# Kernel optimization log

Hardware: AMD Instinct MI355X
Metric: run time of the kernel (lower is better)

Reference implementation:

```python
import jax, jax.numpy as jnp
import numpy as np

NUM_HEADS = 8
EMBED_DIM = 512
MAX_SEQ = 2048
HEAD_DIM = EMBED_DIM // NUM_HEADS
B, S = 2, 2048


def setup_inputs() -> dict:
    key = jax.random.key(0)
    ks = jax.random.split(key, 12)
    sd = 1.0 / np.sqrt(EMBED_DIM)
    return {
        "q_in": jax.random.normal(ks[0], (B, S, EMBED_DIM), jnp.float32),
        "k_in": jax.random.normal(ks[1], (B, S, EMBED_DIM), jnp.float32),
        "v_in": jax.random.normal(ks[2], (B, S, EMBED_DIM), jnp.float32),
        "Wq": jax.random.normal(ks[3], (EMBED_DIM, EMBED_DIM), jnp.float32) * sd,
        "bq": jnp.zeros((EMBED_DIM,), jnp.float32),
        "Wk": jax.random.normal(ks[4], (EMBED_DIM, EMBED_DIM), jnp.float32) * sd,
        "bk": jnp.zeros((EMBED_DIM,), jnp.float32),
        "Wv": jax.random.normal(ks[5], (EMBED_DIM, EMBED_DIM), jnp.float32) * sd,
        "bv": jnp.zeros((EMBED_DIM,), jnp.float32),
        "Wo": jax.random.normal(ks[6], (EMBED_DIM, EMBED_DIM), jnp.float32) * sd,
        "bo": jnp.zeros((EMBED_DIM,), jnp.float32),
        "rel_emb": jax.random.normal(ks[7], (MAX_SEQ, HEAD_DIM), jnp.float32) * sd,
    }


def _split_heads(x, W, b):
    # x: [B,S,E] -> [B,H,S,D]
    y = x @ W + b
    b_, s_ = y.shape[0], y.shape[1]
    return y.reshape(b_, s_, NUM_HEADS, HEAD_DIM).transpose(0, 2, 1, 3)


def _relative_scores(q, rel_emb):
    # q: [B,H,L,D]; rel_emb sliced to last L rows: [M,D] with M == L here
    L = q.shape[2]
    rel = rel_emb[max(0, MAX_SEQ - L):, :]
    M = rel.shape[0]
    scores = jnp.einsum('bhld,md->bhlm', q, rel)
    # mask = flip(tri(L,M), axis=-1): zero out future relative positions
    mask = jnp.flip(jnp.tri(L, M, dtype=jnp.float32), axis=1)
    scores = scores * mask
    # skew trick: pad one column on the left, reshape swapping last two dims, drop first row
    padded = jnp.pad(scores, ((0, 0), (0, 0), (0, 0), (1, 0)))  # [B,H,L,M+1]
    reshaped = padded.reshape(padded.shape[0], padded.shape[1], M + 1, L)
    skewed = reshaped[:, :, 1:, :]  # [B,H,M,L] == [B,H,L,L]
    return skewed


def reference(q_in, k_in, v_in, Wq, bq, Wk, bk, Wv, bv, Wo, bo, rel_emb):
    q = _split_heads(q_in, Wq, bq)  # [B,H,S,D]
    k = _split_heads(k_in, Wk, bk)
    v = _split_heads(v_in, Wv, bv)
    scores = jnp.einsum('bhqd,bhkd->bhqk', q, k)
    rel_scores = _relative_scores(q, rel_emb)
    logits = (scores + rel_scores) / jnp.sqrt(jnp.float32(HEAD_DIM))
    attn = jax.nn.softmax(logits, axis=-1)
    out = jnp.einsum('bhqk,bhkd->bhqd', attn, v)  # [B,H,S,D]
    merged = out.transpose(0, 2, 1, 3).reshape(out.shape[0], -1, EMBED_DIM)
    return merged @ Wo + bo, attn
```

## Files before the change

kernel.cpp:

```cpp
#include <hip/hip_runtime.h>


typedef __attribute__((ext_vector_type(4))) float f32x4;
typedef __attribute__((ext_vector_type(8))) short short8;

__device__ inline unsigned short f2bf(float x) {
    unsigned u = __float_as_uint(x);
    unsigned r = (u + 0x7fffu + ((u >> 16) & 1u)) >> 16;
    return (unsigned short)r;
}
__device__ inline float bf2f(unsigned short h) {
    return __uint_as_float(((unsigned)h) << 16);
}
__device__ inline int swz(int row, int bytecol) {
    return (row << 7) + (bytecol ^ ((row & 7) << 4));
}
__device__ inline void cvt4(float4 v, uint2& hi, uint2& lo) {
    unsigned short h0 = f2bf(v.x), h1 = f2bf(v.y), h2 = f2bf(v.z), h3 = f2bf(v.w);
    hi = make_uint2(((unsigned)h1 << 16) | h0, ((unsigned)h3 << 16) | h2);
    lo = make_uint2(((unsigned)f2bf(v.y - bf2f(h1)) << 16) | f2bf(v.x - bf2f(h0)),
                    ((unsigned)f2bf(v.w - bf2f(h3)) << 16) | f2bf(v.z - bf2f(h2)));
}
__device__ inline uint2 cvt4hi(float4 v) {
    return make_uint2(((unsigned)f2bf(v.y) << 16) | f2bf(v.x),
                      ((unsigned)f2bf(v.w) << 16) | f2bf(v.z));
}

__global__ __launch_bounds__(256) void wt_prep4(const float* __restrict__ W0,
                                                const float* __restrict__ W1,
                                                const float* __restrict__ W2,
                                                const float* __restrict__ W3,
                                                unsigned short* __restrict__ wt)
{
    __shared__ float Ls[32][33];
    const int t = threadIdx.x;
    const int z = blockIdx.z;
    const float* W = (z == 0) ? W0 : (z == 1) ? W1 : (z == 2) ? W2 : W3;
    unsigned short* WTh = wt + (size_t)(2 * z) * 262144;
    unsigned short* WTl = wt + (size_t)(2 * z + 1) * 262144;
    const int k0 = blockIdx.x << 5, n0 = blockIdx.y << 5;
#pragma unroll
    for (int i = 0; i < 4; ++i) {
        int idx = (i << 8) + t;
        int kk = idx >> 5, nn = idx & 31;
        Ls[kk][nn] = W[(size_t)(k0 + kk) * 512 + n0 + nn];
    }
    __syncthreads();
#pragma unroll
    for (int i = 0; i < 2; ++i) {
        int idx = (i << 8) + t;
        int nn = idx >> 4, kp = idx & 15;
        float f0 = Ls[2 * kp][nn], f1 = Ls[2 * kp + 1][nn];
        unsigned short h0 = f2bf(f0), h1 = f2bf(f1);
        size_t off = (size_t)(n0 + nn) * 512 + k0 + 2 * kp;
        *(unsigned*)&WTh[off] = ((unsigned)h1 << 16) | h0;
        *(unsigned*)&WTl[off] = ((unsigned)f2bf(f1 - bf2f(h1)) << 16) | f2bf(f0 - bf2f(h0));
    }
}

__global__ __launch_bounds__(256) void rel_prep(const float* __restrict__ rel,
                                                unsigned short* __restrict__ relh)
{
    int idx = (blockIdx.x * 256 + threadIdx.x) << 3;
    float4 a = *(const float4*)&rel[idx];
    float4 b = *(const float4*)&rel[idx + 4];
    uint4 o;
    o.x = ((unsigned)f2bf(a.y) << 16) | f2bf(a.x);
    o.y = ((unsigned)f2bf(a.w) << 16) | f2bf(a.z);
    o.z = ((unsigned)f2bf(b.y) << 16) | f2bf(b.x);
    o.w = ((unsigned)f2bf(b.w) << 16) | f2bf(b.z);
    *(uint4*)&relh[idx] = o;
}

__device__ __forceinline__ void gemm64_core(const float* __restrict__ A,
                                            const unsigned short* __restrict__ WTh,
                                            const unsigned short* __restrict__ WTl,
                                            int m0, int n0, char* smem, int t,
                                            f32x4 (&acc)[4])
{
    char* aH = smem;
    char* aL = smem + 8192;
    char* wH = smem + 16384;
    char* wL = smem + 24576;
    const int lane = t & 63, w = t >> 6;
    const int lr = lane & 15, kg = lane >> 4;

    for (int k0 = 0; k0 < 512; k0 += 64) {
        if (k0) __syncthreads();
#pragma unroll
        for (int i = 0; i < 4; ++i) {
            int idx = (i << 8) + t;
            int row = idx >> 4, c4 = idx & 15;
            float4 v = *(const float4*)&A[(size_t)(m0 + row) * 512 + k0 + (c4 << 2)];
            uint2 hi, lo; cvt4(v, hi, lo);
            int ph = swz(row, c4 << 3);
            *(uint2*)(aH + ph) = hi;
            *(uint2*)(aL + ph) = lo;
        }
#pragma unroll
        for (int i = 0; i < 4; ++i) {
            int idx = (i << 8) + t;
            int plane = idx >> 9, rem = idx & 511;
            int nn = rem >> 3, j8 = rem & 7;
            const unsigned short* src = plane ? WTl : WTh;
            uint4 vv = *(const uint4*)&src[(size_t)(n0 + nn) * 512 + k0 + (j8 << 3)];
            *(uint4*)((plane ? wL : wH) + swz(nn, j8 << 4)) = vv;
        }
        __syncthreads();
#pragma unroll
        for (int kk = 0; kk < 2; ++kk) {
            int bc = (kk << 6) + (kg << 4);
            int ar = (w << 4) + lr;
            short8 a_h = *(const short8*)(aH + swz(ar, bc));
            short8 a_l = *(const short8*)(aL + swz(ar, bc));
#pragma unroll
            for (int f = 0; f < 4; ++f) {
                short8 b_h = *(const short8*)(wH + swz((f << 4) + lr, bc));
                short8 b_l = *(const short8*)(wL + swz((f << 4) + lr, bc));
                acc[f] = __builtin_amdgcn_mfma_f32_16x16x32_bf16(a_h, b_h, acc[f], 0, 0, 0);
                acc[f] = __builtin_amdgcn_mfma_f32_16x16x32_bf16(a_l, b_h, acc[f], 0, 0, 0);
                acc[f] = __builtin_amdgcn_mfma_f32_16x16x32_bf16(a_h, b_l, acc[f], 0, 0, 0);
            }
        }
    }
}

__global__ __launch_bounds__(256) void gemm_qkv(
    const float* __restrict__ Aq, const float* __restrict__ Ak, const float* __restrict__ Av,
    const unsigned short* __restrict__ wt,
    const float* __restrict__ bq, const float* __restrict__ bk, const float* __restrict__ bv,
    unsigned short* __restrict__ qh, unsigned short* __restrict__ ql,
    unsigned short* __restrict__ kh, unsigned short* __restrict__ kl,
    unsigned short* __restrict__ vh, unsigned short* __restrict__ vl)
{
    __shared__ char smem[32768];
    const int t = threadIdx.x;
    const int z = blockIdx.z;
    const int n0 = blockIdx.x << 6;
    const int m0 = blockIdx.y << 6;
    const int lane = t & 63, w = t >> 6;
    const int lr = lane & 15, kg = lane >> 4;

    const float* A = (z == 0) ? Aq : (z == 1) ? Ak : Av;
    const float* bias = (z == 0) ? bq : (z == 1) ? bk : bv;
    const unsigned short* WTh = wt + (size_t)(2 * z) * 262144;
    const unsigned short* WTl = wt + (size_t)(2 * z + 1) * 262144;
    unsigned short* outH = (z == 0) ? qh : (z == 1) ? kh : vh;
    unsigned short* outL = (z == 0) ? ql : (z == 1) ? kl : vl;

    f32x4 acc[4];
#pragma unroll
    for (int f = 0; f < 4; ++f) acc[f] = {0.f, 0.f, 0.f, 0.f};

    gemm64_core(A, WTh, WTl, m0, n0, smem, t, acc);

    const int mbase = m0 + (w << 4) + (kg << 2);
    const int b = mbase >> 11, s = mbase & 2047;
    const int bidx = (b << 3) + (n0 >> 6);
#pragma unroll
    for (int f = 0; f < 4; ++f) {
        int d = (f << 4) + lr;
        float bv_ = bias[n0 + d];
        if (z < 2) {
#pragma unroll
            for (int e = 0; e < 4; ++e) {
                float val = acc[f][e] + bv_;
                unsigned short hh = f2bf(val);
                size_t off = ((size_t)bidx * 2048 + s + e) * 64 + d;
                outH[off] = hh;
                outL[off] = f2bf(val - bf2f(hh));
            }
        } else {
            unsigned short h[4], l[4];
#pragma unroll
            for (int e = 0; e < 4; ++e) {
                float val = acc[f][e] + bv_;
                h[e] = f2bf(val);
                l[e] = f2bf(val - bf2f(h[e]));
            }
            size_t off = ((size_t)bidx * 64 + d) * 2048 + s;
            *(uint2*)&outH[off] = make_uint2(((unsigned)h[1] << 16) | h[0],
                                             ((unsigned)h[3] << 16) | h[2]);
            *(uint2*)&outL[off] = make_uint2(((unsigned)l[1] << 16) | l[0],
                                             ((unsigned)l[3] << 16) | l[2]);
        }
    }
}

__global__ __launch_bounds__(256) void gemm_out(
    const float* __restrict__ pO,
    const unsigned short* __restrict__ WTh, const unsigned short* __restrict__ WTl,
    const float* __restrict__ bias, float* __restrict__ out0)
{
    __shared__ char smem[32768];
    char* aH = smem;
    char* aL = smem + 8192;
    char* wH = smem + 16384;
    char* wL = smem + 24576;
    const int t = threadIdx.x;
    const int n0 = blockIdx.x << 6;
    const int m0 = blockIdx.y << 6;
    const int lane = t & 63, w = t >> 6;
    const int lr = lane & 15, kg = lane >> 4;
    const int bq = m0 >> 11, s0 = m0 & 2047;

    f32x4 acc[4];
#pragma unroll
    for (int f = 0; f < 4; ++f) acc[f] = {0.f, 0.f, 0.f, 0.f};

    for (int k0 = 0; k0 < 512; k0 += 64) {
        if (k0) __syncthreads();
        const float* p0 = pO + ((size_t)((bq << 3) + (k0 >> 6)) * 2048 + s0) * 64;
#pragma unroll
        for (int i = 0; i < 2; ++i) {
            int idx = (i << 8) + t;
            int row = idx >> 3, j8 = idx & 7;
            size_t off = (size_t)row * 64 + (j8 << 3);
            float4 a0 = *(const float4*)&p0[off];
            float4 a1 = *(const float4*)&p0[off + 4];
            float4 b0 = *(const float4*)&p0[off + 2097152];
            float4 b1 = *(const float4*)&p0[off + 4 + 2097152];
            float4 v0 = make_float4(a0.x + b0.x, a0.y + b0.y, a0.z + b0.z, a0.w + b0.w);
            float4 v1 = make_float4(a1.x + b1.x, a1.y + b1.y, a1.z + b1.z, a1.w + b1.w);
            uint2 h0, l0, h1, l1;
            cvt4(v0, h0, l0);
            cvt4(v1, h1, l1);
            int ph = swz(row, j8 << 4);
            *(uint4*)(aH + ph) = make_uint4(h0.x, h0.y, h1.x, h1.y);
            *(uint4*)(aL + ph) = make_uint4(l0.x, l0.y, l1.x, l1.y);
        }
#pragma unroll
        for (int i = 0; i < 4; ++i) {
            int idx = (i << 8) + t;
            int plane = idx >> 9, rem = idx & 511;
            int nn = rem >> 3, j8 = rem & 7;
            const unsigned short* src = plane ? WTl : WTh;
            uint4 vv = *(const uint4*)&src[(size_t)(n0 + nn) * 512 + k0 + (j8 << 3)];
            *(uint4*)((plane ? wL : wH) + swz(nn, j8 << 4)) = vv;
        }
        __syncthreads();
#pragma unroll
        for (int kk = 0; kk < 2; ++kk) {
            int bc = (kk << 6) + (kg << 4);
            int ar = (w << 4) + lr;
            short8 a_h = *(const short8*)(aH + swz(ar, bc));
            short8 a_l = *(const short8*)(aL + swz(ar, bc));
#pragma unroll
            for (int f = 0; f < 4; ++f) {
                short8 b_h = *(const short8*)(wH + swz((f << 4) + lr, bc));
                short8 b_l = *(const short8*)(wL + swz((f << 4) + lr, bc));
                acc[f] = __builtin_amdgcn_mfma_f32_16x16x32_bf16(a_h, b_h, acc[f], 0, 0, 0);
                acc[f] = __builtin_amdgcn_mfma_f32_16x16x32_bf16(a_l, b_h, acc[f], 0, 0, 0);
                acc[f] = __builtin_amdgcn_mfma_f32_16x16x32_bf16(a_h, b_l, acc[f], 0, 0, 0);
            }
        }
    }

    const int mbase = m0 + (w << 4) + (kg << 2);
#pragma unroll
    for (int f = 0; f < 4; ++f) {
        int n = n0 + (f << 4) + lr;
        float bv = bias[n];
#pragma unroll
        for (int e = 0; e < 4; ++e)
            out0[(size_t)(mbase + e) * 512 + n] = acc[f][e] + bv;
    }
}

__global__ __launch_bounds__(512, 4) void logits_flash(
    const unsigned short* __restrict__ qh_g, const unsigned short* __restrict__ ql_g,
    const unsigned short* __restrict__ kh_g, const unsigned short* __restrict__ kl_g,
    const unsigned short* __restrict__ relh_g,
    float* __restrict__ attn, unsigned short* __restrict__ rawh,
    float* __restrict__ tilemax, int mode,
    float2* __restrict__ stats)
{
    __shared__ char smem[59136];
    char* kh = smem;
    char* kl = smem + 16384;
    char* bandP = smem + 32768;
    unsigned short* Pt = (unsigned short*)(smem + 32768);
    float* part_m = (float*)(smem + 58112);
    float* part_z = (float*)(smem + 58624);

    const int t = threadIdx.x;
    const int bh = blockIdx.y;
    int ib = blockIdx.x; if (bh & 8) ib = 31 - ib;
    const int i0 = ib << 6;
    const int lane = t & 63, w = t >> 6;
    const int wr = w >> 1, wc = w & 1;
    const int lr = lane & 15, kg = lane >> 4;
    const int irow = (wr << 4) + lr;

    const size_t qoff = ((size_t)bh * 2048 + i0 + irow) * 64;
    const short8 aH0 = *(const short8*)(qh_g + qoff + (kg << 3));
    const short8 aH1 = *(const short8*)(qh_g + qoff + 32 + (kg << 3));
    const short8 aL0 = *(const short8*)(ql_g + qoff + (kg << 3));
    const short8 aL1 = *(const short8*)(ql_g + qoff + 32 + (kg << 3));

    float rm = -3.0e38f, rz = 0.f;

    const unsigned short* khb = kh_g + (size_t)bh * 2048 * 64;
    const unsigned short* klb = kl_g + (size_t)bh * 2048 * 64;
    const size_t obase = ((size_t)bh * 2048 + i0) * 2048;

    for (int jt = 0; jt < 16; ++jt) {
        const int j0 = jt << 7;
        const bool anyRel = (j0 <= i0 + 63);
        const int m0 = 1984 - i0 + j0;
        __syncthreads();
        if (jt > 0 && t < 64) {
            float m1 = part_m[t], m2 = part_m[64 + t];
            float z1 = part_z[t], z2 = part_z[64 + t];
            float tm = fmaxf(m1, m2);
            float tz = z1 * __expf((m1 - tm) * 0.125f) + z2 * __expf((m2 - tm) * 0.125f);
            float mn = fmaxf(rm, tm);
            rz = rz * __expf((rm - mn) * 0.125f) + tz * __expf((tm - mn) * 0.125f);
            rm = mn;
        }
        {
            int rr = t >> 2, gp = (t & 3) << 1;
            const unsigned short* s0 = khb + (size_t)(j0 + rr) * 64 + (gp << 3);
            *(uint4*)(kh + swz(rr, gp << 4)) = *(const uint4*)s0;
            *(uint4*)(kh + swz(rr, (gp + 1) << 4)) = *(const uint4*)(s0 + 8);
            const unsigned short* s1 = klb + (size_t)(j0 + rr) * 64 + (gp << 3);
            *(uint4*)(kl + swz(rr, gp << 4)) = *(const uint4*)s1;
            *(uint4*)(kl + swz(rr, (gp + 1) << 4)) = *(const uint4*)(s1 + 8);
        }
        if (anyRel) {
#pragma unroll
            for (int i = 0; i < 3; ++i) {
                int idx = (i << 9) + t;
                int row = idx >> 3, g = idx & 7;
                int m = m0 + row; if (m > 2047) m = 2047;
                *(uint4*)(bandP + swz(row, g << 4)) = *(const uint4*)(relh_g + (size_t)m * 64 + (g << 3));
            }
        }
        __syncthreads();

        f32x4 acc[4];
#pragma unroll
        for (int cf = 0; cf < 4; ++cf) {
            int krow = (wc << 6) + (cf << 4) + lr;
            short8 bH0 = *(const short8*)(kh + swz(krow, kg << 4));
            short8 bH1 = *(const short8*)(kh + swz(krow, 64 + (kg << 4)));
            short8 bL0 = *(const short8*)(kl + swz(krow, kg << 4));
            short8 bL1 = *(const short8*)(kl + swz(krow, 64 + (kg << 4)));
            f32x4 c = {0.f, 0.f, 0.f, 0.f};
            c = __builtin_amdgcn_mfma_f32_16x16x32_bf16(bH0, aH0, c, 0, 0, 0);
            c = __builtin_amdgcn_mfma_f32_16x16x32_bf16(bH1, aH1, c, 0, 0, 0);
            c = __builtin_amdgcn_mfma_f32_16x16x32_bf16(bH0, aL0, c, 0, 0, 0);
            c = __builtin_amdgcn_mfma_f32_16x16x32_bf16(bH1, aL1, c, 0, 0, 0);
            c = __builtin_amdgcn_mfma_f32_16x16x32_bf16(bL0, aH0, c, 0, 0, 0);
            c = __builtin_amdgcn_mfma_f32_16x16x32_bf16(bL1, aH1, c, 0, 0, 0);
            acc[cf] = c;
        }
        if (anyRel) {
            f32x4 pr[6];
#pragma unroll
            for (int q = 0; q < 6; ++q) {
                int ff = (wc ? 6 : 0) + q;
                int brow = (ff << 4) + lr;
                short8 rb0 = *(const short8*)(bandP + swz(brow, kg << 4));
                short8 rb1 = *(const short8*)(bandP + swz(brow, 64 + (kg << 4)));
                f32x4 c = {0.f, 0.f, 0.f, 0.f};
                c = __builtin_amdgcn_mfma_f32_16x16x32_bf16(rb0, aH0, c, 0, 0, 0);
                c = __builtin_amdgcn_mfma_f32_16x16x32_bf16(rb1, aH1, c, 0, 0, 0);
                pr[q] = c;
            }
            __syncthreads();
#pragma unroll
            for (int q = 0; q < 6; ++q) {
                int ff = (wc ? 6 : 0) + q;
#pragma unroll
                for (int e = 0; e < 4; ++e)
                    Pt[((ff << 4) + (kg << 2) + e) * 66 + irow] = f2bf(pr[q][e]);
            }
            __syncthreads();
        }

        float rowmax = -3.0e38f;
#pragma unroll
        for (int cf = 0; cf < 4; ++cf) {
            int jl0 = (wc << 6) + (cf << 4) + (kg << 2);
            f32x4 a = acc[cf];
#pragma unroll
            for (int e = 0; e < 4; ++e) {
                int jl = jl0 + e;
                if (anyRel && (jl - irow) <= (i0 - j0))
                    a[e] += bf2f(Pt[(jl + 63 - irow) * 66 + irow]);
            }
            acc[cf] = a;
            rowmax = fmaxf(rowmax, fmaxf(fmaxf(a[0], a[1]), fmaxf(a[2], a[3])));
        }
        rowmax = fmaxf(rowmax, __shfl_xor(rowmax, 16, 64));
        rowmax = fmaxf(rowmax, __shfl_xor(rowmax, 32, 64));

        float zs = 0.f;
#pragma unroll
        for (int cf = 0; cf < 4; ++cf) {
            int jl0 = (wc << 6) + (cf << 4) + (kg << 2);
            f32x4 a = acc[cf];
            f32x4 u;
#pragma unroll
            for (int e = 0; e < 4; ++e) {
                u[e] = __expf((a[e] - rowmax) * 0.125f);
                zs += u[e];
            }
            size_t oidx = obase + (size_t)irow * 2048 + j0 + jl0;
            if (mode == 2) {
                *(uint2*)&rawh[oidx] = make_uint2(
                    (unsigned)f2bf(u[0]) | ((unsigned)f2bf(u[1]) << 16),
                    (unsigned)f2bf(u[2]) | ((unsigned)f2bf(u[3]) << 16));
            } else if (mode == 1) {
                *(uint2*)&rawh[oidx] = make_uint2(
                    (unsigned)f2bf(a[0]) | ((unsigned)f2bf(a[1]) << 16),
                    (unsigned)f2bf(a[2]) | ((unsigned)f2bf(a[3]) << 16));
            } else {
                *(float4*)&attn[oidx] = make_float4(a[0], a[1], a[2], a[3]);
            }
        }
        zs += __shfl_xor(zs, 16, 64);
        zs += __shfl_xor(zs, 32, 64);
        if (lane < 16) {
            part_m[(wc << 6) + irow] = rowmax;
            part_z[(wc << 6) + irow] = zs;
            if (mode == 2)
                tilemax[(size_t)((jt << 1) + wc) * 32768 + bh * 2048 + i0 + irow] = rowmax;
        }
    }
    __syncthreads();
    if (t < 64) {
        float m1 = part_m[t], m2 = part_m[64 + t];
        float z1 = part_z[t], z2 = part_z[64 + t];
        float tm = fmaxf(m1, m2);
        float tz = z1 * __expf((m1 - tm) * 0.125f) + z2 * __expf((m2 - tm) * 0.125f);
        float mn = fmaxf(rm, tm);
        rz = rz * __expf((rm - mn) * 0.125f) + tz * __expf((tm - mn) * 0.125f);
        rm = mn;
        stats[bh * 2048 + i0 + t] = make_float2(rm, 1.0f / rz);
    }
}

__global__ __launch_bounds__(256) void pv_fused(float* __restrict__ attn,
                                                const unsigned short* __restrict__ rawh,
                                                const float* __restrict__ tilemax, int mode,
                                                const unsigned short* __restrict__ vTh,
                                                const unsigned short* __restrict__ vTl,
                                                const float2* __restrict__ stats,
                                                float* __restrict__ pO)
{
    __shared__ char smem[25088];
    char* pH = smem;
    char* vH = smem + 8192;
    char* vL = smem + 16384;
    float2* sm = (float2*)(smem + 24576);

    const int t = threadIdx.x;
    const int i0 = blockIdx.x << 6;
    const int bh = blockIdx.y;
    const int jc = blockIdx.z;
    const int jc0 = jc << 10;
    const int lane = t & 63, w = t >> 6;
    const int lr = lane & 15, kg = lane >> 4;

    float* ab = attn + ((size_t)bh * 2048 + i0) * 2048;
    const unsigned short* rb = rawh + ((size_t)bh * 2048 + i0) * 2048;
    const unsigned short* vhb = vTh + (size_t)bh * 64 * 2048;
    const unsigned short* vlb = vTl + (size_t)bh * 64 * 2048;
    const int tmbase = bh * 2048 + i0;

    if (t < 64) sm[t] = stats[bh * 2048 + i0 + t];
    __syncthreads();

    f32x4 acc[4];
#pragma unroll
    for (int f = 0; f < 4; ++f) acc[f] = {0.f, 0.f, 0.f, 0.f};

    for (int j0 = jc0; j0 < jc0 + 1024; j0 += 64) {
        if (j0 != jc0) __syncthreads();
        const int half = j0 >> 6;
#pragma unroll
        for (int i = 0; i < 4; ++i) {
            int idx = (i << 8) + t;
            int row = idx >> 4, c4 = idx & 15;
            size_t go = (size_t)row * 2048 + j0 + (c4 << 2);
            float2 s2 = sm[row];
            float4 p;
            if (mode == 2) {
                uint2 rv = *(const uint2*)&rb[go];
                float corr = __expf((tilemax[(size_t)half * 32768 + tmbase + row] - s2.x) * 0.125f) * s2.y;
                p.x = bf2f((unsigned short)(rv.x & 0xffff)) * corr;
                p.y = bf2f((unsigned short)(rv.x >> 16)) * corr;
                p.z = bf2f((unsigned short)(rv.y & 0xffff)) * corr;
                p.w = bf2f((unsigned short)(rv.y >> 16)) * corr;
            } else {
                float4 x;
                if (mode == 1) {
                    uint2 rv = *(const uint2*)&rb[go];
                    x = make_float4(bf2f((unsigned short)(rv.x & 0xffff)),
                                    bf2f((unsigned short)(rv.x >> 16)),
                                    bf2f((unsigned short)(rv.y & 0xffff)),
                                    bf2f((unsigned short)(rv.y >> 16)));
                } else {
                    x = *(const float4*)&ab[go];
                }
                p.x = __expf((x.x - s2.x) * 0.125f) * s2.y;
                p.y = __expf((x.y - s2.x) * 0.125f) * s2.y;
                p.z = __expf((x.z - s2.x) * 0.125f) * s2.y;
                p.w = __expf((x.w - s2.x) * 0.125f) * s2.y;
            }
            *(float4*)&ab[go] = p;
            *(uint2*)(pH + swz(row, c4 << 3)) = cvt4hi(p);
        }
#pragma unroll
        for (int i = 0; i < 4; ++i) {
            int idx = (i << 8) + t;
            int plane = idx >> 9, rem = idx & 511;
            int d = rem >> 3, g8 = rem & 7;
            const unsigned short* src = (plane ? vlb : vhb) + (size_t)d * 2048 + j0 + (g8 << 3);
            *(uint4*)((plane ? vL : vH) + swz(d, g8 << 4)) = *(const uint4*)src;
        }
        __syncthreads();
#pragma unroll
        for (int kk = 0; kk < 2; ++kk) {
            int bc = (kk << 6) + (kg << 4);
            int ar = (w << 4) + lr;
            short8 a_h = *(const short8*)(pH + swz(ar, bc));
#pragma unroll
            for (int f = 0; f < 4; ++f) {
                short8 b_h = *(const short8*)(vH + swz((f << 4) + lr, bc));
                short8 b_l = *(const short8*)(vL + swz((f << 4) + lr, bc));
                acc[f] = __builtin_amdgcn_mfma_f32_16x16x32_bf16(a_h, b_h, acc[f], 0, 0, 0);
                acc[f] = __builtin_amdgcn_mfma_f32_16x16x32_bf16(a_h, b_l, acc[f], 0, 0, 0);
            }
        }
    }
#pragma unroll
    for (int f = 0; f < 4; ++f) {
#pragma unroll
        for (int e = 0; e < 4; ++e) {
            int m = i0 + (w << 4) + (kg << 2) + e;
            pO[(size_t)jc * 2097152 + ((size_t)bh * 2048 + m) * 64 + (f << 4) + lr] = acc[f][e];
        }
    }
}

extern "C" void kernel_launch(void* const* d_in, const int* in_sizes, int n_in,
                              void* d_out, int out_size, void* d_ws, size_t ws_size,
                              hipStream_t stream)
{
    const float* q_in = (const float*)d_in[0];
    const float* k_in = (const float*)d_in[1];
    const float* v_in = (const float*)d_in[2];
    const float* Wq   = (const float*)d_in[3];
    const float* bq   = (const float*)d_in[4];
    const float* Wk   = (const float*)d_in[5];
    const float* bk   = (const float*)d_in[6];
    const float* Wv   = (const float*)d_in[7];
    const float* bv   = (const float*)d_in[8];
    const float* Wo   = (const float*)d_in[9];
    const float* bo   = (const float*)d_in[10];
    const float* rel  = (const float*)d_in[11];

    float* out0 = (float*)d_out;
    float* attn = out0 + 2097152;

    float* ws = (float*)d_ws;
    unsigned short* qh = (unsigned short*)ws;
    unsigned short* ql = qh + 2097152;
    unsigned short* kh = (unsigned short*)(ws + 2097152);
    unsigned short* kl = kh + 2097152;
    unsigned short* vTh = (unsigned short*)(ws + 4194304);
    unsigned short* vTl = vTh + 2097152;
    unsigned short* wt = (unsigned short*)(ws + 6291456);
    unsigned short* relh = (unsigned short*)(ws + 7340032);
    float2* stats = (float2*)(ws + 7405568);
    unsigned short* rawh = (unsigned short*)(ws + 7471104);
    float* tilemax = ws + 41025536;
    float* pO = ws;

    const int mode = (ws_size >= 168296448ULL) ? 2
                   : (ws_size >= 164102144ULL) ? 1 : 0;

    wt_prep4<<<dim3(16, 16, 4), 256, 0, stream>>>(Wq, Wk, Wv, Wo, wt);
    rel_prep<<<64, 256, 0, stream>>>(rel, relh);

    gemm_qkv<<<dim3(8, 64, 3), 256, 0, stream>>>(q_in, k_in, v_in, wt,
                                                 bq, bk, bv,
                                                 qh, ql, kh, kl, vTh, vTl);

    logits_flash<<<dim3(32, 16), 512, 0, stream>>>(qh, ql, kh, kl, relh,
                                                   attn, rawh, tilemax, mode, stats);
    pv_fused<<<dim3(32, 16, 2), 256, 0, stream>>>(attn, rawh, tilemax, mode,
                                                  vTh, vTl, stats, pO);

    gemm_out<<<dim3(8, 64), 256, 0, stream>>>(pO,
                                              wt + 6 * 262144, wt + 7 * 262144,
                                              bo, out0);
}
```

Measured before the change: 320.1 us.

## Split attention-probability writeback out of PV kernel into a separate streaming pass

Removes the float4 write of the normalized attention matrix from the PV matmul kernel and moves it into a new norm_stream kernel launched after the output GEMM. Each row is processed by one wavefront, which recomputes the normalized probabilities from the raw logits and writes them with coalesced stores. The PV kernel becomes lighter and purely compute-oriented. In exchange the raw logits are read a second time and there is an extra kernel launch.

```diff
diff --git a/kernel.cpp b/kernel.cpp
--- a/kernel.cpp
+++ b/kernel.cpp
@@ -442,13 +442,13 @@
     }
 }
 
-__global__ __launch_bounds__(256) void pv_fused(float* __restrict__ attn,
-                                                const unsigned short* __restrict__ rawh,
-                                                const float* __restrict__ tilemax, int mode,
-                                                const unsigned short* __restrict__ vTh,
-                                                const unsigned short* __restrict__ vTl,
-                                                const float2* __restrict__ stats,
-                                                float* __restrict__ pO)
+__global__ __launch_bounds__(256) void pv_mm(const float* __restrict__ attn,
+                                             const unsigned short* __restrict__ rawh,
+                                             const float* __restrict__ tilemax, int mode,
+                                             const unsigned short* __restrict__ vTh,
+                                             const unsigned short* __restrict__ vTl,
+                                             const float2* __restrict__ stats,
+                                             float* __restrict__ pO)
 {
     __shared__ char smem[25088];
     char* pH = smem;
@@ -464,7 +464,7 @@
     const int lane = t & 63, w = t >> 6;
     const int lr = lane & 15, kg = lane >> 4;
 
-    float* ab = attn + ((size_t)bh * 2048 + i0) * 2048;
+    const float* ab = attn + ((size_t)bh * 2048 + i0) * 2048;
     const unsigned short* rb = rawh + ((size_t)bh * 2048 + i0) * 2048;
     const unsigned short* vhb = vTh + (size_t)bh * 64 * 2048;
     const unsigned short* vlb = vTl + (size_t)bh * 64 * 2048;
@@ -510,7 +510,6 @@
                 p.z = __expf((x.z - s2.x) * 0.125f) * s2.y;
                 p.w = __expf((x.w - s2.x) * 0.125f) * s2.y;
             }
-            *(float4*)&ab[go] = p;
             *(uint2*)(pH + swz(row, c4 << 3)) = cvt4hi(p);
         }
 #pragma unroll
@@ -543,6 +542,49 @@
             int m = i0 + (w << 4) + (kg << 2) + e;
             pO[(size_t)jc * 2097152 + ((size_t)bh * 2048 + m) * 64 + (f << 4) + lr] = acc[f][e];
         }
+    }
+}
+
+__global__ __launch_bounds__(256) void norm_stream(float* __restrict__ attn,
+                                                   const unsigned short* __restrict__ rawh,
+                                                   const float* __restrict__ tilemax, int mode,
+                                                   const float2* __restrict__ stats)
+{
+    const int t = threadIdx.x;
+    const int lane = t & 63, w = t >> 6;
+    const int row = (blockIdx.x << 2) + w;
+    const float2 s2 = stats[row];
+    float* arow = attn + (size_t)row * 2048;
+    const unsigned short* urow = rawh + (size_t)row * 2048;
+
+#pragma unroll
+    for (int c = 0; c < 8; ++c) {
+        int col = (c << 8) + (lane << 2);
+        float4 p;
+        if (mode == 2) {
+            uint2 rv = *(const uint2*)&urow[col];
+            float corr = __expf((tilemax[(size_t)(col >> 6) * 32768 + row] - s2.x) * 0.125f) * s2.y;
+            p.x = bf2f((unsigned short)(rv.x & 0xffff)) * corr;
+            p.y = bf2f((unsigned short)(rv.x >> 16)) * corr;
+            p.z = bf2f((unsigned short)(rv.y & 0xffff)) * corr;
+            p.w = bf2f((unsigned short)(rv.y >> 16)) * corr;
+        } else {
+            float4 x;
+            if (mode == 1) {
+                uint2 rv = *(const uint2*)&urow[col];
+                x = make_float4(bf2f((unsigned short)(rv.x & 0xffff)),
+                                bf2f((unsigned short)(rv.x >> 16)),
+                                bf2f((unsigned short)(rv.y & 0xffff)),
+                                bf2f((unsigned short)(rv.y >> 16)));
+            } else {
+                x = *(const float4*)&arow[col];
+            }
+            p.x = __expf((x.x - s2.x) * 0.125f) * s2.y;
+            p.y = __expf((x.y - s2.x) * 0.125f) * s2.y;
+            p.z = __expf((x.z - s2.x) * 0.125f) * s2.y;
+            p.w = __expf((x.w - s2.x) * 0.125f) * s2.y;
+        }
+        *(float4*)&arow[col] = p;
     }
 }
 
@@ -592,10 +634,10 @@
 
     logits_flash<<<dim3(32, 16), 512, 0, stream>>>(qh, ql, kh, kl, relh,
                                                    attn, rawh, tilemax, mode, stats);
-    pv_fused<<<dim3(32, 16, 2), 256, 0, stream>>>(attn, rawh, tilemax, mode,
-                                                  vTh, vTl, stats, pO);
-
+    pv_mm<<<dim3(32, 16, 2), 256, 0, stream>>>(attn, rawh, tilemax, mode,
+                                               vTh, vTl, stats, pO);
     gemm_out<<<dim3(8, 64), 256, 0, stream>>>(pO,
                                               wt + 6 * 262144, wt + 7 * 262144,
                                               bo, out0);
-}
+    norm_stream<<<8192, 256, 0, stream>>>(attn, rawh, tilemax, mode, stats);
+}
```

After: 325.3 us. About the same (+1.6%).
